# Kernel tuning notes

Hardware: AMD Instinct MI355X
Metric: run time of the kernel (lower is better)

The kernel has to match this reference:

```python
import jax, jax.numpy as jnp
import numpy as np

B, N, C, H = 2, 2048, 512, 8
D = C // H  # head dim = 64
SCALE = C ** -0.5  # module uses heads_channels**-0.5 (full inner dim, not per-head)


def setup_inputs() -> dict:
    key = jax.random.key(0)
    ks = jax.random.split(key, 9)
    return {
        "q": jax.random.normal(ks[0], (B, N, C), jnp.float32),
        "kv": jax.random.normal(ks[1], (B, N, C), jnp.float32),
        "pos_q": jax.random.normal(ks[2], (B, N, D), jnp.float32),
        "pos_k": jax.random.normal(ks[3], (B, N, D), jnp.float32),
        "Wq": jax.random.normal(ks[4], (C, C), jnp.float32) * (C ** -0.5),
        "Wk": jax.random.normal(ks[5], (C, C), jnp.float32) * (C ** -0.5),
        "Wv": jax.random.normal(ks[6], (C, C), jnp.float32) * (C ** -0.5),
        "Wo": jax.random.normal(ks[7], (C, C), jnp.float32) * (C ** -0.5),
        "bo": jnp.zeros((C,), jnp.float32),
    }


def reference(q, kv, pos_q, pos_k, Wq, Wk, Wv, Wo, bo):
    # projections: [b n c] @ [c c] -> [b n c]
    qp = q @ Wq
    kp = kv @ Wk
    vp = kv @ Wv
    # split heads: b n (h d) -> b h n d
    split = lambda t: t.reshape(B, N, H, D).transpose(0, 2, 1, 3)
    qh, kh, vh = split(qp), split(kp), split(vp)
    # additive positional bias, broadcast over heads: b n d -> b 1 n d
    qh = qh + pos_q[:, None, :, :]
    kh = kh + pos_k[:, None, :, :]
    sim = jnp.einsum("bhid,bhjd->bhij", qh, kh) * SCALE
    attn = jax.nn.softmax(sim, axis=-1)
    out = jnp.einsum("bhij,bhjd->bhid", attn, vh)
    # merge heads: b h n d -> b n (h d)
    out = out.transpose(0, 2, 1, 3).reshape(B, N, C)
    return out @ Wo + bo
```

## Files before the change

kernel.cpp:

```cpp
#include <hip/hip_runtime.h>
#include <hip/hip_bf16.h>
#include <stdint.h>
#include <math.h>

static constexpr int kB = 2, kN = 2048, kC = 512, kH = 8, kD = 64;
static constexpr float kScaleL2E =
    (float)(0.044194173824159216 * 1.4426950408889634);
static constexpr float kShift = 12.0f;
static constexpr int kSplit = 4;
static constexpr size_t kSegF = (size_t)kB * kN * kC;

typedef short bf16x8 __attribute__((ext_vector_type(8)));
typedef short bf16x4 __attribute__((ext_vector_type(4)));
typedef float f32x4  __attribute__((ext_vector_type(4)));

__device__ __forceinline__ float bf2f(unsigned short u) {
  union { unsigned int i; float f; } v; v.i = ((unsigned int)u) << 16; return v.f;
}
__device__ __forceinline__ unsigned short f2bf(float f) {
  union { float f; unsigned int i; } v; v.f = f;
  unsigned int x = v.i;
  return (unsigned short)((x + 0x7FFFu + ((x >> 16) & 1u)) >> 16);
}
__device__ __forceinline__ short f2bs(float f) { return (short)f2bf(f); }
__device__ __forceinline__ unsigned int pack2_t(float lo, float hi) {
  union { float f; unsigned int i; } a, b; a.f = lo; b.f = hi;
  return (b.i & 0xFFFF0000u) | (a.i >> 16);
}

__global__ __launch_bounds__(256) void prep_kernel(
    const float* __restrict__ q, const float* __restrict__ kv,
    const float* __restrict__ Wq, const float* __restrict__ Wk,
    const float* __restrict__ Wv,
    unsigned short* __restrict__ qbf, unsigned short* __restrict__ kvbf,
    unsigned short* __restrict__ wT)
{
  const int t = threadIdx.x;
  if (blockIdx.z == 0) {
    const int gid = blockIdx.x * 256 + t;
    #pragma unroll
    for (int it = 0; it < 8; ++it) {
      int i4 = gid + it * 65536;
      float4 a = *(const float4*)(q + (size_t)i4 * 4);
      float4 b = *(const float4*)(kv + (size_t)i4 * 4);
      bf16x4 ab = {f2bs(a.x), f2bs(a.y), f2bs(a.z), f2bs(a.w)};
      bf16x4 bb = {f2bs(b.x), f2bs(b.y), f2bs(b.z), f2bs(b.w)};
      *(bf16x4*)(qbf + (size_t)i4 * 4) = ab;
      *(bf16x4*)(kvbf + (size_t)i4 * 4) = bb;
    }
  } else {
    if (blockIdx.x >= 192) return;
    const int wsel = blockIdx.x >> 6;
    const int tile = blockIdx.x & 63;
    const int tr = tile >> 3, tc = tile & 7;
    const float* W = (wsel == 0) ? Wq : (wsel == 1 ? Wk : Wv);
    unsigned short* out = wT + (size_t)wsel * kC * kC;

    __shared__ __align__(16) float Ts[64][68];
    #pragma unroll
    for (int it = 0; it < 4; ++it) {
      int e = t + it * 256;
      int r = e >> 4, c4 = (e & 15) * 4;
      *(float4*)&Ts[r][c4] =
          *(const float4*)(W + (size_t)(tr * 64 + r) * kC + tc * 64 + c4);
    }
    __syncthreads();
    const int n = t >> 2, ks = (t & 3) * 16;
    unsigned short* orow = out + (size_t)(tc * 64 + n) * kC + tr * 64 + ks;
    #pragma unroll
    for (int c = 0; c < 4; ++c) {
      ushort4 o;
      o.x = f2bf(Ts[ks + c * 4 + 0][n]);
      o.y = f2bf(Ts[ks + c * 4 + 1][n]);
      o.z = f2bf(Ts[ks + c * 4 + 2][n]);
      o.w = f2bf(Ts[ks + c * 4 + 3][n]);
      *(ushort4*)(orow + c * 4) = o;
    }
  }
}

__global__ __launch_bounds__(256) void proj_kernel(
    const unsigned short* __restrict__ qbf,
    const unsigned short* __restrict__ kvbf,
    const unsigned short* __restrict__ wT,
    const float* __restrict__ pos_q,
    const float* __restrict__ pos_k,
    unsigned short* __restrict__ qh,
    unsigned short* __restrict__ kh,
    unsigned short* __restrict__ vhT)
{
  const bool kvmode = (blockIdx.z == 1);
  const unsigned short* A = kvmode ? kvbf : qbf;
  const unsigned short* Bt0 = wT + (kvmode ? (size_t)kC * kC : 0);
  const unsigned short* Bt1 = wT + 2 * (size_t)kC * kC;

  __shared__ __align__(16) unsigned short As[128][72];
  __shared__ __align__(16) unsigned short Bs[2][64][72];

  const int t = threadIdx.x;
  const int w = t >> 6, lane = t & 63;
  const int l15 = lane & 15, quad = lane >> 4;
  const int m0 = blockIdx.x * 128;
  const int n0 = blockIdx.y * 64;

  const int sr = t >> 3, sc = (t & 7) * 8;

  bf16x8 pa[4], pb0[2], pb1[2];
  #pragma unroll
  for (int i = 0; i < 4; ++i)
    pa[i] = *(const bf16x8*)(A + (size_t)(m0 + sr + i * 32) * kC + sc);
  #pragma unroll
  for (int i = 0; i < 2; ++i)
    pb0[i] = *(const bf16x8*)(Bt0 + (size_t)(n0 + sr + i * 32) * kC + sc);
  if (kvmode)
    #pragma unroll
    for (int i = 0; i < 2; ++i)
      pb1[i] = *(const bf16x8*)(Bt1 + (size_t)(n0 + sr + i * 32) * kC + sc);

  f32x4 acc0[2][4], acc1[2][4];
  #pragma unroll
  for (int si = 0; si < 2; ++si)
    #pragma unroll
    for (int ct = 0; ct < 4; ++ct) {
      acc0[si][ct] = (f32x4){0.f, 0.f, 0.f, 0.f};
      acc1[si][ct] = (f32x4){0.f, 0.f, 0.f, 0.f};
    }

  for (int k0 = 0; k0 < kC; k0 += 64) {
    if (k0) __syncthreads();
    #pragma unroll
    for (int i = 0; i < 4; ++i) *(bf16x8*)&As[sr + i * 32][sc] = pa[i];
    #pragma unroll
    for (int i = 0; i < 2; ++i) *(bf16x8*)&Bs[0][sr + i * 32][sc] = pb0[i];
    if (kvmode)
      #pragma unroll
      for (int i = 0; i < 2; ++i) *(bf16x8*)&Bs[1][sr + i * 32][sc] = pb1[i];
    __syncthreads();
    if (k0 + 64 < kC) {
      int kn = k0 + 64;
      #pragma unroll
      for (int i = 0; i < 4; ++i)
        pa[i] = *(const bf16x8*)(A + (size_t)(m0 + sr + i * 32) * kC + kn + sc);
      #pragma unroll
      for (int i = 0; i < 2; ++i)
        pb0[i] = *(const bf16x8*)(Bt0 + (size_t)(n0 + sr + i * 32) * kC + kn + sc);
      if (kvmode)
        #pragma unroll
        for (int i = 0; i < 2; ++i)
          pb1[i] = *(const bf16x8*)(Bt1 + (size_t)(n0 + sr + i * 32) * kC + kn + sc);
    }
    bf16x8 a0[2], a1[2];
    #pragma unroll
    for (int si = 0; si < 2; ++si) {
      a0[si] = *(const bf16x8*)&As[w * 32 + si * 16 + l15][quad * 8];
      a1[si] = *(const bf16x8*)&As[w * 32 + si * 16 + l15][32 + quad * 8];
    }
    #pragma unroll
    for (int ct = 0; ct < 4; ++ct) {
      bf16x8 b0 = *(const bf16x8*)&Bs[0][ct * 16 + l15][quad * 8];
      bf16x8 b1 = *(const bf16x8*)&Bs[0][ct * 16 + l15][32 + quad * 8];
      #pragma unroll
      for (int si = 0; si < 2; ++si) {
        acc0[si][ct] = __builtin_amdgcn_mfma_f32_16x16x32_bf16(a0[si], b0, acc0[si][ct], 0, 0, 0);
        acc0[si][ct] = __builtin_amdgcn_mfma_f32_16x16x32_bf16(a1[si], b1, acc0[si][ct], 0, 0, 0);
      }
      if (kvmode) {
        bf16x8 c0 = *(const bf16x8*)&Bs[1][ct * 16 + l15][quad * 8];
        bf16x8 c1 = *(const bf16x8*)&Bs[1][ct * 16 + l15][32 + quad * 8];
        #pragma unroll
        for (int si = 0; si < 2; ++si) {
          acc1[si][ct] = __builtin_amdgcn_mfma_f32_16x16x32_bf16(a0[si], c0, acc1[si][ct], 0, 0, 0);
          acc1[si][ct] = __builtin_amdgcn_mfma_f32_16x16x32_bf16(a1[si], c1, acc1[si][ct], 0, 0, 0);
        }
      }
    }
  }

  const int h = n0 >> 6;
  if (!kvmode) {
    #pragma unroll
    for (int si = 0; si < 2; ++si)
      #pragma unroll
      for (int r = 0; r < 4; ++r) {
        int m = m0 + w * 32 + si * 16 + quad * 4 + r;
        int b = m >> 11, n_seq = m & (kN - 1);
        #pragma unroll
        for (int ct = 0; ct < 4; ++ct) {
          int d = ct * 16 + l15;
          float val = (acc0[si][ct][r] +
                       pos_q[((size_t)b * kN + n_seq) * kD + d]) * kScaleL2E;
          qh[(((size_t)b * kH + h) * kN + n_seq) * kD + d] = f2bf(val);
        }
      }
  } else {
    #pragma unroll
    for (int si = 0; si < 2; ++si)
      #pragma unroll
      for (int r = 0; r < 4; ++r) {
        int m = m0 + w * 32 + si * 16 + quad * 4 + r;
        int b = m >> 11, n_seq = m & (kN - 1);
        #pragma unroll
        for (int ct = 0; ct < 4; ++ct) {
          int d = ct * 16 + l15;
          float vk = acc0[si][ct][r] + pos_k[((size_t)b * kN + n_seq) * kD + d];
          kh[(((size_t)b * kH + h) * kN + n_seq) * kD + d] = f2bf(vk);
        }
      }
    __syncthreads();
    unsigned short (*Tv)[136] = (unsigned short(*)[136])&As[0][0];
    #pragma unroll
    for (int si = 0; si < 2; ++si)
      #pragma unroll
      for (int ct = 0; ct < 4; ++ct) {
        const int d = ct * 16 + l15;
        const int nl = w * 32 + si * 16 + quad * 4;
        unsigned int lo = (unsigned int)f2bf(acc1[si][ct][0]) |
                          ((unsigned int)f2bf(acc1[si][ct][1]) << 16);
        unsigned int hi = (unsigned int)f2bf(acc1[si][ct][2]) |
                          ((unsigned int)f2bf(acc1[si][ct][3]) << 16);
        *(unsigned int*)&Tv[d][nl]     = lo;
        *(unsigned int*)&Tv[d][nl + 2] = hi;
      }
    __syncthreads();
    const int c16 = t & 15, dr = t >> 4;
    const int b2 = m0 >> 11, nbase = m0 & (kN - 1);
    #pragma unroll
    for (int rep = 0; rep < 4; ++rep) {
      const int d = rep * 16 + dr;
      bf16x8 vv = *(const bf16x8*)&Tv[d][c16 * 8];
      *(bf16x8*)(vhT + (((size_t)(b2 * kH + h)) * kD + d) * kN + nbase + c16 * 8) = vv;
    }
  }
}

__global__ __launch_bounds__(256, 4) void attn_kernel(
    const unsigned short* __restrict__ qh,
    const unsigned short* __restrict__ kh,
    const unsigned short* __restrict__ vhT,
    unsigned short* __restrict__ opart,
    float* __restrict__ lbuf)
{
  const int bh = blockIdx.y;
  const int b = bh >> 3, h = bh & 7;
  const int q0 = blockIdx.x * 128;
  const int s = blockIdx.z;
  const int kbase = s * (kN / kSplit);
  const int nkt = kN / kSplit / 64;
  const int t = threadIdx.x;
  const int w = t >> 6, lane = t & 63;
  const int l15 = lane & 15, quad = lane >> 4;

  __shared__ __align__(16) unsigned short Kbf[2][64][72];
  __shared__ __align__(16) unsigned short Vt[2][64][72];

  const unsigned short* Qb = qh  + (size_t)bh * kN * kD;
  const unsigned short* Kb = kh  + (size_t)bh * kN * kD;
  const unsigned short* Vb = vhT + (size_t)bh * kD * kN;

  bf16x8 aq[2][2];
  #pragma unroll
  for (int g = 0; g < 2; ++g) {
    const unsigned short* qrow = Qb + (size_t)(q0 + w * 32 + g * 16 + l15) * kD;
    aq[g][0] = *(const bf16x8*)(qrow + quad * 8);
    aq[g][1] = *(const bf16x8*)(qrow + 32 + quad * 8);
  }

  const int sr = t >> 3, sc = (t & 7) * 8, sr2 = sr + 32;

  bf16x8 pk0 = *(const bf16x8*)(Kb + (size_t)(kbase + sr) * kD + sc);
  bf16x8 pk1 = *(const bf16x8*)(Kb + (size_t)(kbase + sr2) * kD + sc);
  bf16x8 pv0 = *(const bf16x8*)(Vb + (size_t)sr * kN + kbase + sc);
  bf16x8 pv1 = *(const bf16x8*)(Vb + (size_t)sr2 * kN + kbase + sc);
  *(bf16x8*)&Kbf[0][sr][sc]  = pk0;
  *(bf16x8*)&Kbf[0][sr2][sc] = pk1;
  *(bf16x8*)&Vt[0][sr][sc]   = pv0;
  *(bf16x8*)&Vt[0][sr2][sc]  = pv1;
  {
    int kt1 = kbase + 64;
    pk0 = *(const bf16x8*)(Kb + (size_t)(kt1 + sr) * kD + sc);
    pk1 = *(const bf16x8*)(Kb + (size_t)(kt1 + sr2) * kD + sc);
    pv0 = *(const bf16x8*)(Vb + (size_t)sr * kN + kt1 + sc);
    pv1 = *(const bf16x8*)(Vb + (size_t)sr2 * kN + kt1 + sc);
  }

  f32x4 o[2][4];
  #pragma unroll
  for (int g = 0; g < 2; ++g)
    #pragma unroll
    for (int nt = 0; nt < 4; ++nt) o[g][nt] = (f32x4){0.f, 0.f, 0.f, 0.f};
  float l_run[2] = {0.f, 0.f};

  const int src_a = l15 + 32 * (quad & 1);
  const int src_b = src_a + 16;
  const bool hi_sel = (quad & 2) != 0;

  for (int i = 0; i < nkt; ++i) {
    __syncthreads();
    if (i + 1 < nkt) {
      unsigned short (*Kw)[72] = Kbf[(i + 1) & 1];
      unsigned short (*Vw)[72] = Vt[(i + 1) & 1];
      *(bf16x8*)&Kw[sr][sc]  = pk0;
      *(bf16x8*)&Kw[sr2][sc] = pk1;
      *(bf16x8*)&Vw[sr][sc]  = pv0;
      *(bf16x8*)&Vw[sr2][sc] = pv1;
      if (i + 2 < nkt) {
        int ktn = kbase + (i + 2) * 64;
        pk0 = *(const bf16x8*)(Kb + (size_t)(ktn + sr) * kD + sc);
        pk1 = *(const bf16x8*)(Kb + (size_t)(ktn + sr2) * kD + sc);
        pv0 = *(const bf16x8*)(Vb + (size_t)sr * kN + ktn + sc);
        pv1 = *(const bf16x8*)(Vb + (size_t)sr2 * kN + ktn + sc);
      }
    }
    const unsigned short (*Kr)[72] = Kbf[i & 1];
    const unsigned short (*Vr)[72] = Vt[i & 1];

    f32x4 sacc[2][4];
    __builtin_amdgcn_s_setprio(1);
    #pragma unroll
    for (int ct = 0; ct < 4; ++ct) {
      bf16x8 ak0 = *(const bf16x8*)&Kr[ct * 16 + l15][quad * 8];
      bf16x8 ak1 = *(const bf16x8*)&Kr[ct * 16 + l15][32 + quad * 8];
      #pragma unroll
      for (int g = 0; g < 2; ++g) {
        f32x4 zz = (f32x4){0.f, 0.f, 0.f, 0.f};
        zz = __builtin_amdgcn_mfma_f32_16x16x32_bf16(ak0, aq[g][0], zz, 0, 0, 0);
        zz = __builtin_amdgcn_mfma_f32_16x16x32_bf16(ak1, aq[g][1], zz, 0, 0, 0);
        sacc[g][ct] = zz;
      }
    }
    __builtin_amdgcn_s_setprio(0);

    union PF { unsigned int u[4]; bf16x8 v; } pf[2][2];
    #pragma unroll
    for (int g = 0; g < 2; ++g) {
      float psum = 0.f;
      #pragma unroll
      for (int ct = 0; ct < 4; ++ct)
        #pragma unroll
        for (int r = 0; r < 4; ++r) {
          float p = exp2f(sacc[g][ct][r] - kShift);
          sacc[g][ct][r] = p;
          psum += p;
        }
      psum += __shfl_xor(psum, 16);
      psum += __shfl_xor(psum, 32);
      l_run[g] += psum;

      unsigned int pk01[4], pk23[4];
      #pragma unroll
      for (int ct = 0; ct < 4; ++ct) {
        pk01[ct] = pack2_t(sacc[g][ct][0], sacc[g][ct][1]);
        pk23[ct] = pack2_t(sacc[g][ct][2], sacc[g][ct][3]);
      }
      unsigned int s01a[4], s23a[4], s01b[4], s23b[4];
      #pragma unroll
      for (int ct = 0; ct < 4; ++ct) {
        s01a[ct] = (unsigned int)__shfl((int)pk01[ct], src_a);
        s23a[ct] = (unsigned int)__shfl((int)pk23[ct], src_a);
        s01b[ct] = (unsigned int)__shfl((int)pk01[ct], src_b);
        s23b[ct] = (unsigned int)__shfl((int)pk23[ct], src_b);
      }
      pf[g][0].u[0] = hi_sel ? s01a[1] : s01a[0];
      pf[g][0].u[1] = hi_sel ? s23a[1] : s23a[0];
      pf[g][0].u[2] = hi_sel ? s01b[1] : s01b[0];
      pf[g][0].u[3] = hi_sel ? s23b[1] : s23b[0];
      pf[g][1].u[0] = hi_sel ? s01a[3] : s01a[2];
      pf[g][1].u[1] = hi_sel ? s23a[3] : s23a[2];
      pf[g][1].u[2] = hi_sel ? s01b[3] : s01b[2];
      pf[g][1].u[3] = hi_sel ? s23b[3] : s23b[2];
    }

    __builtin_amdgcn_s_setprio(1);
    #pragma unroll
    for (int nt = 0; nt < 4; ++nt) {
      bf16x8 av0 = *(const bf16x8*)&Vr[nt * 16 + l15][quad * 8];
      bf16x8 av1 = *(const bf16x8*)&Vr[nt * 16 + l15][32 + quad * 8];
      #pragma unroll
      for (int g = 0; g < 2; ++g) {
        o[g][nt] = __builtin_amdgcn_mfma_f32_16x16x32_bf16(av0, pf[g][0].v, o[g][nt], 0, 0, 0);
        o[g][nt] = __builtin_amdgcn_mfma_f32_16x16x32_bf16(av1, pf[g][1].v, o[g][nt], 0, 0, 0);
      }
    }
    __builtin_amdgcn_s_setprio(0);
  }

  if (quad == 0)
    #pragma unroll
    for (int g = 0; g < 2; ++g)
      lbuf[(size_t)(s * 16 + bh) * kN + q0 + w * 32 + g * 16 + l15] = l_run[g];

  __syncthreads();
  unsigned short (*Ot)[72] = (unsigned short(*)[72])&Kbf[0][0][0];
  #pragma unroll
  for (int g = 0; g < 2; ++g) {
    const int ql = w * 32 + g * 16 + l15;
    #pragma unroll
    for (int nt = 0; nt < 4; ++nt) {
      unsigned int lo = (unsigned int)f2bf(o[g][nt][0]) |
                        ((unsigned int)f2bf(o[g][nt][1]) << 16);
      unsigned int hi = (unsigned int)f2bf(o[g][nt][2]) |
                        ((unsigned int)f2bf(o[g][nt][3]) << 16);
      const int d0 = nt * 16 + quad * 4;
      *(unsigned int*)&Ot[ql][d0]     = lo;
      *(unsigned int*)&Ot[ql][d0 + 2] = hi;
    }
  }
  __syncthreads();
  {
    unsigned short* od = opart + (size_t)s * kSegF;
    const int c8 = t & 7, qb = t >> 3;
    #pragma unroll
    for (int rep = 0; rep < 4; ++rep) {
      const int ql = rep * 32 + qb;
      bf16x8 vv = *(const bf16x8*)&Ot[ql][c8 * 8];
      *(bf16x8*)(od + ((size_t)b * kN + (q0 + ql)) * kC + h * kD + c8 * 8) = vv;
    }
  }
}

__global__ __launch_bounds__(256) void proj_out_kernel(
    const unsigned short* __restrict__ opart,
    const float* __restrict__ lbuf,
    const float* __restrict__ Wo,
    const float* __restrict__ bo,
    float* __restrict__ out)
{
  __shared__ __align__(16) unsigned short Wt[64][72];

  const int t = threadIdx.x;
  const int w = t >> 6, lane = t & 63;
  const int l15 = lane & 15, quad = lane >> 4;
  const int m0 = blockIdx.x * 64;
  const int n0 = blockIdx.y * 64;

  const int m = m0 + w * 16 + l15;
  const int nseq = m & (kN - 1);
  const int bb = m >> 11;
  const size_t arow = (size_t)m * kC;

  ushort4 pw[4];
  #pragma unroll
  for (int i = 0; i < 4; ++i) {
    int e = t + i * 256;
    int r = e >> 4, c4 = (e & 15) * 4;
    float4 wv = *(const float4*)(Wo + (size_t)r * kC + n0 + c4);
    pw[i] = make_ushort4(f2bf(wv.x), f2bf(wv.y), f2bf(wv.z), f2bf(wv.w));
  }

  f32x4 acc[4];
  #pragma unroll
  for (int ct = 0; ct < 4; ++ct) acc[ct] = (f32x4){0.f, 0.f, 0.f, 0.f};

  #pragma unroll
  for (int k0 = 0; k0 < kC; k0 += 64) {
    if (k0) __syncthreads();
    #pragma unroll
    for (int i = 0; i < 4; ++i) {
      int e = t + i * 256;
      int r = e >> 4, c4 = (e & 15) * 4;
      Wt[c4 + 0][r] = pw[i].x;
      Wt[c4 + 1][r] = pw[i].y;
      Wt[c4 + 2][r] = pw[i].z;
      Wt[c4 + 3][r] = pw[i].w;
    }
    __syncthreads();

    const int h = k0 >> 6;
    const int bh = bb * 8 + h;
    float lsum = 0.f;
    #pragma unroll
    for (int s = 0; s < kSplit; ++s)
      lsum += lbuf[(size_t)(s * 16 + bh) * kN + nseq];
    const float wgt = 1.f / lsum;

    float af0[8] = {}, af1[8] = {};
    #pragma unroll
    for (int s = 0; s < kSplit; ++s) {
      bf16x8 v0 = *(const bf16x8*)(opart + (size_t)s * kSegF + arow + k0 + quad * 8);
      bf16x8 v1 = *(const bf16x8*)(opart + (size_t)s * kSegF + arow + k0 + 32 + quad * 8);
      #pragma unroll
      for (int j = 0; j < 8; ++j) {
        af0[j] += bf2f((unsigned short)v0[j]);
        af1[j] += bf2f((unsigned short)v1[j]);
      }
    }
    bf16x8 a0, a1;
    #pragma unroll
    for (int j = 0; j < 8; ++j) {
      a0[j] = (short)f2bf(af0[j] * wgt);
      a1[j] = (short)f2bf(af1[j] * wgt);
    }

    if (k0 + 64 < kC) {
      int kn = k0 + 64;
      #pragma unroll
      for (int i = 0; i < 4; ++i) {
        int e = t + i * 256;
        int r = e >> 4, c4 = (e & 15) * 4;
        float4 wv = *(const float4*)(Wo + (size_t)(kn + r) * kC + n0 + c4);
        pw[i] = make_ushort4(f2bf(wv.x), f2bf(wv.y), f2bf(wv.z), f2bf(wv.w));
      }
    }
    #pragma unroll
    for (int ct = 0; ct < 4; ++ct) {
      bf16x8 b0 = *(const bf16x8*)&Wt[ct * 16 + l15][quad * 8];
      bf16x8 b1 = *(const bf16x8*)&Wt[ct * 16 + l15][32 + quad * 8];
      acc[ct] = __builtin_amdgcn_mfma_f32_16x16x32_bf16(a0, b0, acc[ct], 0, 0, 0);
      acc[ct] = __builtin_amdgcn_mfma_f32_16x16x32_bf16(a1, b1, acc[ct], 0, 0, 0);
    }
  }

  #pragma unroll
  for (int ct = 0; ct < 4; ++ct) {
    int n = n0 + ct * 16 + l15;
    float bb2 = bo[n];
    #pragma unroll
    for (int r = 0; r < 4; ++r) {
      int mm = m0 + w * 16 + quad * 4 + r;
      out[(size_t)mm * kC + n] = acc[ct][r] + bb2;
    }
  }
}

extern "C" void kernel_launch(void* const* d_in, const int* in_sizes, int n_in,
                              void* d_out, int out_size, void* d_ws, size_t ws_size,
                              hipStream_t stream) {
  (void)in_sizes; (void)n_in; (void)out_size; (void)ws_size;
  const float* q     = (const float*)d_in[0];
  const float* kv    = (const float*)d_in[1];
  const float* pos_q = (const float*)d_in[2];
  const float* pos_k = (const float*)d_in[3];
  const float* Wq    = (const float*)d_in[4];
  const float* Wk    = (const float*)d_in[5];
  const float* Wv    = (const float*)d_in[6];
  const float* Wo    = (const float*)d_in[7];
  const float* bo    = (const float*)d_in[8];
  float* out = (float*)d_out;

  const size_t seg = (size_t)kB * kH * kN * kD;

  unsigned short* qbf  = (unsigned short*)d_ws;
  unsigned short* kvbf = qbf + seg;
  unsigned short* wT   = kvbf + seg;
  unsigned short* qhp  = wT + 3 * (size_t)kC * kC;
  unsigned short* khp  = qhp + seg;
  unsigned short* vtp  = khp + seg;
  unsigned short* opart = vtp + seg;
  float* lbuf = (float*)(opart + (size_t)kSplit * kSegF);

  dim3 blk(256);
  prep_kernel<<<dim3(256, 1, 2), blk, 0, stream>>>(q, kv, Wq, Wk, Wv, qbf, kvbf, wT);
  proj_kernel<<<dim3(32, 8, 2), blk, 0, stream>>>(qbf, kvbf, wT, pos_q, pos_k,
                                                  qhp, khp, vtp);
  attn_kernel<<<dim3(16, 16, kSplit), blk, 0, stream>>>(qhp, khp, vtp, opart, lbuf);
  proj_out_kernel<<<dim3(64, 8), blk, 0, stream>>>(opart, lbuf, Wo, bo, out);
}
```

Baseline: 157.8 us.

## Feed P directly from S accumulators via 16x16x16 MFMA and permuted V layout

Removes the cross-lane shuffle and select sequence that rearranged the softmax probabilities into the B-operand layout of the 16x16x32 MFMA. Instead, P accumulator registers are packed in place and used as B operands of 16x16x16 bf16 MFMAs. V tiles are written to shared memory in a permuted column order so that each lane's A operands line up with that register layout. The cost is twice as many MFMA instructions, each with a smaller K, in exchange for fewer ds_bpermute/shuffle operations and fewer VALU selects.

```diff
diff --git a/kernel.cpp b/kernel.cpp
--- a/kernel.cpp
+++ b/kernel.cpp
@@ -26,6 +26,14 @@
 __device__ __forceinline__ unsigned int pack2_t(float lo, float hi) {
   union { float f; unsigned int i; } a, b; a.f = lo; b.f = hi;
   return (b.i & 0xFFFF0000u) | (a.i >> 16);
+}
+
+__device__ __forceinline__ f32x4 mfma16(bf16x4 a, bf16x4 b, f32x4 c) {
+#if __has_builtin(__builtin_amdgcn_mfma_f32_16x16x16_bf16)
+  return __builtin_amdgcn_mfma_f32_16x16x16_bf16(a, b, c, 0, 0, 0);
+#else
+  return __builtin_amdgcn_mfma_f32_16x16x16bf16_1k(a, b, c, 0, 0, 0);
+#endif
 }
 
 __global__ __launch_bounds__(256) void prep_kernel(
@@ -266,6 +274,7 @@
   }
 
   const int sr = t >> 3, sc = (t & 7) * 8, sr2 = sr + 32;
+  const int vc0 = ((sc >> 2) & 3) * 16 + (sc >> 4) * 4;
 
   bf16x8 pk0 = *(const bf16x8*)(Kb + (size_t)(kbase + sr) * kD + sc);
   bf16x8 pk1 = *(const bf16x8*)(Kb + (size_t)(kbase + sr2) * kD + sc);
@@ -273,8 +282,16 @@
   bf16x8 pv1 = *(const bf16x8*)(Vb + (size_t)sr2 * kN + kbase + sc);
   *(bf16x8*)&Kbf[0][sr][sc]  = pk0;
   *(bf16x8*)&Kbf[0][sr2][sc] = pk1;
-  *(bf16x8*)&Vt[0][sr][sc]   = pv0;
-  *(bf16x8*)&Vt[0][sr2][sc]  = pv1;
+  {
+    bf16x4 lo0 = {pv0[0], pv0[1], pv0[2], pv0[3]};
+    bf16x4 hi0 = {pv0[4], pv0[5], pv0[6], pv0[7]};
+    bf16x4 lo1 = {pv1[0], pv1[1], pv1[2], pv1[3]};
+    bf16x4 hi1 = {pv1[4], pv1[5], pv1[6], pv1[7]};
+    *(bf16x4*)&Vt[0][sr][vc0]       = lo0;
+    *(bf16x4*)&Vt[0][sr][vc0 + 16]  = hi0;
+    *(bf16x4*)&Vt[0][sr2][vc0]      = lo1;
+    *(bf16x4*)&Vt[0][sr2][vc0 + 16] = hi1;
+  }
   {
     int kt1 = kbase + 64;
     pk0 = *(const bf16x8*)(Kb + (size_t)(kt1 + sr) * kD + sc);
@@ -289,10 +306,6 @@
     #pragma unroll
     for (int nt = 0; nt < 4; ++nt) o[g][nt] = (f32x4){0.f, 0.f, 0.f, 0.f};
   float l_run[2] = {0.f, 0.f};
-
-  const int src_a = l15 + 32 * (quad & 1);
-  const int src_b = src_a + 16;
-  const bool hi_sel = (quad & 2) != 0;
 
   for (int i = 0; i < nkt; ++i) {
     __syncthreads();
@@ -301,8 +314,14 @@
       unsigned short (*Vw)[72] = Vt[(i + 1) & 1];
       *(bf16x8*)&Kw[sr][sc]  = pk0;
       *(bf16x8*)&Kw[sr2][sc] = pk1;
-      *(bf16x8*)&Vw[sr][sc]  = pv0;
-      *(bf16x8*)&Vw[sr2][sc] = pv1;
+      bf16x4 lo0 = {pv0[0], pv0[1], pv0[2], pv0[3]};
+      bf16x4 hi0 = {pv0[4], pv0[5], pv0[6], pv0[7]};
+      bf16x4 lo1 = {pv1[0], pv1[1], pv1[2], pv1[3]};
+      bf16x4 hi1 = {pv1[4], pv1[5], pv1[6], pv1[7]};
+      *(bf16x4*)&Vw[sr][vc0]       = lo0;
+      *(bf16x4*)&Vw[sr][vc0 + 16]  = hi0;
+      *(bf16x4*)&Vw[sr2][vc0]      = lo1;
+      *(bf16x4*)&Vw[sr2][vc0 + 16] = hi1;
       if (i + 2 < nkt) {
         int ktn = kbase + (i + 2) * 64;
         pk0 = *(const bf16x8*)(Kb + (size_t)(ktn + sr) * kD + sc);
@@ -330,7 +349,7 @@
     }
     __builtin_amdgcn_s_setprio(0);
 
-    union PF { unsigned int u[4]; bf16x8 v; } pf[2][2];
+    union PB { unsigned int u[2]; bf16x4 v; } pb[2][4];
     #pragma unroll
     for (int g = 0; g < 2; ++g) {
       float psum = 0.f;
@@ -345,40 +364,28 @@
       psum += __shfl_xor(psum, 16);
       psum += __shfl_xor(psum, 32);
       l_run[g] += psum;
-
-      unsigned int pk01[4], pk23[4];
       #pragma unroll
       for (int ct = 0; ct < 4; ++ct) {
-        pk01[ct] = pack2_t(sacc[g][ct][0], sacc[g][ct][1]);
-        pk23[ct] = pack2_t(sacc[g][ct][2], sacc[g][ct][3]);
-      }
-      unsigned int s01a[4], s23a[4], s01b[4], s23b[4];
-      #pragma unroll
-      for (int ct = 0; ct < 4; ++ct) {
-        s01a[ct] = (unsigned int)__shfl((int)pk01[ct], src_a);
-        s23a[ct] = (unsigned int)__shfl((int)pk23[ct], src_a);
-        s01b[ct] = (unsigned int)__shfl((int)pk01[ct], src_b);
-        s23b[ct] = (unsigned int)__shfl((int)pk23[ct], src_b);
-      }
-      pf[g][0].u[0] = hi_sel ? s01a[1] : s01a[0];
-      pf[g][0].u[1] = hi_sel ? s23a[1] : s23a[0];
-      pf[g][0].u[2] = hi_sel ? s01b[1] : s01b[0];
-      pf[g][0].u[3] = hi_sel ? s23b[1] : s23b[0];
-      pf[g][1].u[0] = hi_sel ? s01a[3] : s01a[2];
-      pf[g][1].u[1] = hi_sel ? s23a[3] : s23a[2];
-      pf[g][1].u[2] = hi_sel ? s01b[3] : s01b[2];
-      pf[g][1].u[3] = hi_sel ? s23b[3] : s23b[2];
+        pb[g][ct].u[0] = pack2_t(sacc[g][ct][0], sacc[g][ct][1]);
+        pb[g][ct].u[1] = pack2_t(sacc[g][ct][2], sacc[g][ct][3]);
+      }
     }
 
     __builtin_amdgcn_s_setprio(1);
     #pragma unroll
     for (int nt = 0; nt < 4; ++nt) {
-      bf16x8 av0 = *(const bf16x8*)&Vr[nt * 16 + l15][quad * 8];
-      bf16x8 av1 = *(const bf16x8*)&Vr[nt * 16 + l15][32 + quad * 8];
+      bf16x8 av0 = *(const bf16x8*)&Vr[nt * 16 + l15][quad * 16];
+      bf16x8 av1 = *(const bf16x8*)&Vr[nt * 16 + l15][quad * 16 + 8];
+      bf16x4 a_ct0 = {av0[0], av0[1], av0[2], av0[3]};
+      bf16x4 a_ct1 = {av0[4], av0[5], av0[6], av0[7]};
+      bf16x4 a_ct2 = {av1[0], av1[1], av1[2], av1[3]};
+      bf16x4 a_ct3 = {av1[4], av1[5], av1[6], av1[7]};
       #pragma unroll
       for (int g = 0; g < 2; ++g) {
-        o[g][nt] = __builtin_amdgcn_mfma_f32_16x16x32_bf16(av0, pf[g][0].v, o[g][nt], 0, 0, 0);
-        o[g][nt] = __builtin_amdgcn_mfma_f32_16x16x32_bf16(av1, pf[g][1].v, o[g][nt], 0, 0, 0);
+        o[g][nt] = mfma16(a_ct0, pb[g][0].v, o[g][nt]);
+        o[g][nt] = mfma16(a_ct1, pb[g][1].v, o[g][nt]);
+        o[g][nt] = mfma16(a_ct2, pb[g][2].v, o[g][nt]);
+        o[g][nt] = mfma16(a_ct3, pb[g][3].v, o[g][nt]);
       }
     }
     __builtin_amdgcn_s_setprio(0);
```

Measured after the change: 158.9 us. No clear change (+0.7%).
